# Performance work log

Hardware: AMD Instinct MI355X
Metric: run time of the kernel (lower is better)

Reference implementation:

```python
import jax, jax.numpy as jnp
import numpy as np

N, E, D, H, L = 50000, 800000, 64, 4, 2
DH = D // H


def layer_norm(h, g, b, eps=1e-5):
    mu = h.mean(-1, keepdims=True)
    var = ((h - mu) ** 2).mean(-1, keepdims=True)
    return (h - mu) / jnp.sqrt(var + eps) * g + b


def setup_inputs() -> dict:
    key = jax.random.key(0)
    ks = jax.random.split(key, 16)
    s = 1.0 / np.sqrt(D)
    inp = {
        "x": jax.random.normal(ks[0], (N, D), jnp.float32),
        "edge_attr": jax.random.normal(ks[1], (E, D), jnp.float32),
        "edge_index": jax.random.randint(ks[2], (2, E), 0, N, jnp.int64),
        "WQ": jax.random.normal(ks[3], (L, D, D), jnp.float32) * s,
        "WK": jax.random.normal(ks[4], (L, D, D), jnp.float32) * s,
        "WE": jax.random.normal(ks[5], (L, D, D), jnp.float32) * s,
        "WV": jax.random.normal(ks[6], (L, D, D), jnp.float32) * s,
        "WO": jax.random.normal(ks[7], (L, D, D), jnp.float32) * s,
        "bO": jnp.zeros((L, D), jnp.float32),
        "ln1_g": jnp.ones((L, D), jnp.float32),
        "ln1_b": jnp.zeros((L, D), jnp.float32),
        "W1": jax.random.normal(ks[8], (L, D, 2 * D), jnp.float32) * s,
        "b1": jnp.zeros((L, 2 * D), jnp.float32),
        "W2": jax.random.normal(ks[9], (L, 2 * D, D), jnp.float32) * (1.0 / np.sqrt(2 * D)),
        "b2": jnp.zeros((L, D), jnp.float32),
        "ln2_g": jnp.ones((L, D), jnp.float32),
        "ln2_b": jnp.zeros((L, D), jnp.float32),
    }
    return inp


def exphormer_layer(h, edge_attr, src, dst, p):
    (wq, wk, we, wv, wo, bo, g1, be1, w1, b1, w2, b2, g2, be2) = p
    n = h.shape[0]
    Qh = (h @ wq).reshape(n, H, DH)
    Kh = (h @ wk).reshape(n, H, DH)
    Vh = (h @ wv).reshape(n, H, DH)
    Eh = (edge_attr @ we).reshape(-1, H, DH)
    # per-edge score: sum over head_dim of K[src]*Q[dst]*E / sqrt(DH)
    s = jnp.sum(Kh[src] * Qh[dst] * Eh, axis=-1, keepdims=True) / np.sqrt(DH)
    score = jnp.exp(jnp.clip(s, -5.0, 5.0))  # [E, H, 1]
    msg = Vh[src] * score                     # [E, H, DH]
    wV = jax.ops.segment_sum(msg, dst, num_segments=n)    # [N, H, DH]
    Z = jax.ops.segment_sum(score, dst, num_segments=n)   # [N, H, 1]
    h_attn = (wV / (Z + 1e-6)).reshape(n, D)
    h1 = layer_norm(h + (h_attn @ wo + bo), g1, be1)
    ffn = jax.nn.relu(h1 @ w1 + b1) @ w2 + b2
    return layer_norm(h1 + ffn, g2, be2)


def reference(x, edge_attr, edge_index, WQ, WK, WE, WV, WO, bO, ln1_g, ln1_b,
              W1, b1, W2, b2, ln2_g, ln2_b):
    src = edge_index[0]
    dst = edge_index[1]
    h = x
    for l in range(L):
        p = (WQ[l], WK[l], WE[l], WV[l], WO[l], bO[l], ln1_g[l], ln1_b[l],
             W1[l], b1[l], W2[l], b2[l], ln2_g[l], ln2_b[l])
        h = exphormer_layer(h, edge_attr, src, dst, p)
    return h
```

## Files before the change

### kernel.cpp

```cpp
#include <hip/hip_runtime.h>

#define NN 50000
#define NE 800000
#define D  64
#define NL 2
#define NB 196

typedef __bf16 bf16x8 __attribute__((ext_vector_type(8)));
typedef float  floatx4 __attribute__((ext_vector_type(4)));

static __device__ __forceinline__ float bf2f(unsigned short u) {
    return __uint_as_float(((unsigned)u) << 16);
}
static __device__ __forceinline__ unsigned short f2bf(float x) {
    unsigned u = __float_as_uint(x);
    u += 0x7fff + ((u >> 16) & 1);
    return (unsigned short)(u >> 16);
}


__global__ void k_deg(const int* __restrict__ ei, int* __restrict__ deg) {
    int e = blockIdx.x * 256 + threadIdx.x;
    if (e < NE) atomicAdd(&deg[ei[NE + e]], 1);
}

__global__ __launch_bounds__(256) void k_scan1(const int* __restrict__ deg,
                                               int* __restrict__ psum) {
    __shared__ int red[4];
    int i = blockIdx.x * 256 + threadIdx.x;
    int v = (i < NN) ? deg[i] : 0;
#pragma unroll
    for (int m = 1; m < 64; m <<= 1) v += __shfl_xor(v, m, 64);
    if ((threadIdx.x & 63) == 0) red[threadIdx.x >> 6] = v;
    __syncthreads();
    if (threadIdx.x == 0) psum[blockIdx.x] = red[0] + red[1] + red[2] + red[3];
}

__global__ void k_scan2(int* __restrict__ psum) {
    __shared__ int buf[256];
    int t = threadIdx.x;
    int v = (t < NB) ? psum[t] : 0;
    buf[t] = v;
    __syncthreads();
    for (int o = 1; o < 256; o <<= 1) {
        int x = (t >= o) ? buf[t - o] : 0;
        __syncthreads();
        buf[t] += x;
        __syncthreads();
    }
    if (t < NB) psum[t] = buf[t] - v;
}

__global__ __launch_bounds__(256) void k_scan3(const int* __restrict__ deg,
                                               const int* __restrict__ psum,
                                               int* __restrict__ row_off,
                                               int* __restrict__ cursor) {
    __shared__ int buf[256];
    int t = threadIdx.x;
    int i = blockIdx.x * 256 + t;
    int v = (i < NN) ? deg[i] : 0;
    buf[t] = v;
    __syncthreads();
    for (int o = 1; o < 256; o <<= 1) {
        int x = (t >= o) ? buf[t - o] : 0;
        __syncthreads();
        buf[t] += x;
        __syncthreads();
    }
    if (i < NN) {
        int inc = buf[t] + psum[blockIdx.x];
        row_off[i + 1] = inc;
        cursor[i] = inc - v;
        if (i == 0) row_off[0] = 0;
    }
}

__global__ void k_scatter(const int* __restrict__ ei, int* __restrict__ cursor,
                          int* __restrict__ csr_src, int* __restrict__ eperm) {
    int e = blockIdx.x * 256 + threadIdx.x;
    if (e < NE) {
        int dst = ei[NE + e];
        int pos = atomicAdd(&cursor[dst], 1);
        csr_src[pos] = ei[e];
        eperm[e] = pos;
    }
}

__global__ __launch_bounds__(256) void k_prep(
        const float* __restrict__ WQ, const float* __restrict__ WK,
        const float* __restrict__ WV, const float* __restrict__ WE,
        const float* __restrict__ WO, const float* __restrict__ W1,
        const float* __restrict__ W2,
        unsigned short* __restrict__ wqT, unsigned short* __restrict__ wkT,
        unsigned short* __restrict__ wvT, unsigned short* __restrict__ weT,
        unsigned short* __restrict__ woT, unsigned short* __restrict__ w1T,
        unsigned short* __restrict__ w2T) {
    int idx = blockIdx.x * 256 + threadIdx.x;
    if (idx >= 2 * 36864) return;
    int l = idx / 36864;
    int r = idx % 36864;
    if (r < 20480) {
        int which = r >> 12, rr = r & 4095;
        int m = rr >> 6, k = rr & 63;
        const float* src = (which == 0 ? WQ : which == 1 ? WK : which == 2 ? WV :
                            which == 3 ? WE : WO);
        unsigned short* dst = (which == 0 ? wqT : which == 1 ? wkT : which == 2 ? wvT :
                               which == 3 ? weT : woT);
        dst[l * 4096 + rr] = f2bf(src[l * 4096 + k * 64 + m]);
    } else if (r < 28672) {
        int r2 = r - 20480;
        int m = r2 >> 6, k = r2 & 63;
        w1T[l * 8192 + r2] = f2bf(W1[l * 8192 + k * 128 + m]);
    } else {
        int r3 = r - 28672;
        int m = r3 >> 7, k = r3 & 127;
        w2T[l * 8192 + r3] = f2bf(W2[l * 8192 + k * 64 + m]);
    }
}


__global__ __launch_bounds__(256) void k_qkv_mfma(const float* __restrict__ h,
        const unsigned short* __restrict__ wqT, const unsigned short* __restrict__ wkT,
        const unsigned short* __restrict__ wvT,
        unsigned short* __restrict__ Qb, unsigned short* __restrict__ Kb,
        unsigned short* __restrict__ Vb) {
    __shared__ unsigned short st[4][16 * 72];
    const int lane = threadIdx.x & 63;
    const int w    = threadIdx.x >> 6;
    const int ml   = lane & 15;
    const int quad = lane >> 4;

    bf16x8 aq[2][4], ak[2][4], av[2][4];
#pragma unroll
    for (int kt = 0; kt < 2; kt++)
#pragma unroll
        for (int mt = 0; mt < 4; mt++) {
            int o = (mt*16 + ml)*64 + kt*32 + quad*8;
            aq[kt][mt] = *(const bf16x8*)&wqT[o];
            ak[kt][mt] = *(const bf16x8*)&wkT[o];
            av[kt][mt] = *(const bf16x8*)&wvT[o];
        }

    const int wave = blockIdx.x * 4 + w;
    const int nw   = gridDim.x * 4;
    const int el = lane >> 2, c = lane & 3;
    for (int tile = wave; tile < NN / 16; tile += nw) {
        const int e0 = tile * 16;
        const float4* ar = (const float4*)(h + (size_t)(e0 + ml) * D);
        bf16x8 b[2];
#pragma unroll
        for (int kt = 0; kt < 2; kt++) {
            float4 f0 = ar[kt*8 + quad*2 + 0];
            float4 f1 = ar[kt*8 + quad*2 + 1];
            b[kt][0] = (__bf16)f0.x; b[kt][1] = (__bf16)f0.y;
            b[kt][2] = (__bf16)f0.z; b[kt][3] = (__bf16)f0.w;
            b[kt][4] = (__bf16)f1.x; b[kt][5] = (__bf16)f1.y;
            b[kt][6] = (__bf16)f1.z; b[kt][7] = (__bf16)f1.w;
        }
        floatx4 accq[4] = {}, acck[4] = {}, accv[4] = {};
#pragma unroll
        for (int kt = 0; kt < 2; kt++)
#pragma unroll
            for (int mt = 0; mt < 4; mt++) {
                accq[mt] = __builtin_amdgcn_mfma_f32_16x16x32_bf16(aq[kt][mt], b[kt], accq[mt], 0, 0, 0);
                acck[mt] = __builtin_amdgcn_mfma_f32_16x16x32_bf16(ak[kt][mt], b[kt], acck[mt], 0, 0, 0);
                accv[mt] = __builtin_amdgcn_mfma_f32_16x16x32_bf16(av[kt][mt], b[kt], accv[mt], 0, 0, 0);
            }
#pragma unroll
        for (int mt = 0; mt < 4; mt++)
            *(ushort4*)&st[w][ml*72 + mt*16 + quad*4] =
                make_ushort4(f2bf(accq[mt][0]), f2bf(accq[mt][1]),
                             f2bf(accq[mt][2]), f2bf(accq[mt][3]));
        {
            uint4 r0 = *(const uint4*)&st[w][el*72 + c*16 + 0];
            uint4 r1 = *(const uint4*)&st[w][el*72 + c*16 + 8];
            uint4* gp = (uint4*)(Qb + (size_t)(e0 + el) * D + c*16);
            gp[0] = r0; gp[1] = r1;
        }
#pragma unroll
        for (int mt = 0; mt < 4; mt++)
            *(ushort4*)&st[w][ml*72 + mt*16 + quad*4] =
                make_ushort4(f2bf(acck[mt][0]), f2bf(acck[mt][1]),
                             f2bf(acck[mt][2]), f2bf(acck[mt][3]));
        {
            uint4 r0 = *(const uint4*)&st[w][el*72 + c*16 + 0];
            uint4 r1 = *(const uint4*)&st[w][el*72 + c*16 + 8];
            uint4* gp = (uint4*)(Kb + (size_t)(e0 + el) * D + c*16);
            gp[0] = r0; gp[1] = r1;
        }
#pragma unroll
        for (int mt = 0; mt < 4; mt++)
            *(ushort4*)&st[w][ml*72 + mt*16 + quad*4] =
                make_ushort4(f2bf(accv[mt][0]), f2bf(accv[mt][1]),
                             f2bf(accv[mt][2]), f2bf(accv[mt][3]));
        {
            uint4 r0 = *(const uint4*)&st[w][el*72 + c*16 + 0];
            uint4 r1 = *(const uint4*)&st[w][el*72 + c*16 + 8];
            uint4* gp = (uint4*)(Vb + (size_t)(e0 + el) * D + c*16);
            gp[0] = r0; gp[1] = r1;
        }
    }
}

__global__ __launch_bounds__(256) void k_eh_score(const float* __restrict__ ea,
        const unsigned short* __restrict__ weT, const int* __restrict__ eperm,
        const int* __restrict__ ei, const unsigned short* __restrict__ Qb,
        const unsigned short* __restrict__ Kb,
        float* __restrict__ scb, unsigned short* __restrict__ Eh1) {
    __shared__ unsigned short wsm[2 * 4608];
    __shared__ unsigned short st[4][16 * 72];
    const int t = threadIdx.x;
    for (int i = t; i < 1024; i += 256) {
        int l = i >> 9, r = i & 511;
        *(uint4*)&wsm[l*4608 + (r >> 3)*72 + (r & 7)*8] = ((const uint4*)weT)[i];
    }
    __syncthreads();

    const int lane = t & 63;
    const int w    = t >> 6;
    const int ml   = lane & 15;
    const int quad = lane >> 4;
    const int el = lane >> 2, c = lane & 3;
    const int wave = blockIdx.x * 4 + w;
    const int nw   = gridDim.x * 4;
    const int NT   = NE / 16;

    int tile = wave;
    if (tile >= NT) return;
    int srcn = ei[tile*16 + ml];
    int dstn = ei[NE + tile*16 + ml];
    int posm = eperm[tile*16 + ml];

    for (; tile < NT; tile += nw) {
        const float4* ar = (const float4*)(ea + (size_t)(tile*16 + ml) * D);
        float4 f00 = ar[quad*2 + 0];
        float4 f01 = ar[quad*2 + 1];
        float4 f10 = ar[8 + quad*2 + 0];
        float4 f11 = ar[8 + quad*2 + 1];
        ushort4 qg[4], kg[4];
#pragma unroll
        for (int mt = 0; mt < 4; mt++) {
            qg[mt] = *(const ushort4*)(Qb + (size_t)dstn * D + mt*16 + quad*4);
            kg[mt] = *(const ushort4*)(Kb + (size_t)srcn * D + mt*16 + quad*4);
        }
        int nxt = tile + nw;
        int nsrc = srcn, ndst = dstn, nposm = posm;
        if (nxt < NT) {
            nsrc  = ei[nxt*16 + ml];
            ndst  = ei[NE + nxt*16 + ml];
            nposm = eperm[nxt*16 + ml];
        }
        bf16x8 b[2];
        b[0][0] = (__bf16)f00.x; b[0][1] = (__bf16)f00.y;
        b[0][2] = (__bf16)f00.z; b[0][3] = (__bf16)f00.w;
        b[0][4] = (__bf16)f01.x; b[0][5] = (__bf16)f01.y;
        b[0][6] = (__bf16)f01.z; b[0][7] = (__bf16)f01.w;
        b[1][0] = (__bf16)f10.x; b[1][1] = (__bf16)f10.y;
        b[1][2] = (__bf16)f10.z; b[1][3] = (__bf16)f10.w;
        b[1][4] = (__bf16)f11.x; b[1][5] = (__bf16)f11.y;
        b[1][6] = (__bf16)f11.z; b[1][7] = (__bf16)f11.w;

        {
            floatx4 acc[4] = {};
#pragma unroll
            for (int kt = 0; kt < 2; kt++)
#pragma unroll
                for (int mt = 0; mt < 4; mt++) {
                    bf16x8 a = *(const bf16x8*)&wsm[4608 + (mt*16 + ml)*72 + kt*32 + quad*8];
                    acc[mt] = __builtin_amdgcn_mfma_f32_16x16x32_bf16(a, b[kt], acc[mt], 0, 0, 0);
                }
#pragma unroll
            for (int mt = 0; mt < 4; mt++)
                *(ushort4*)&st[w][ml*72 + mt*16 + quad*4] =
                    make_ushort4(f2bf(acc[mt][0]), f2bf(acc[mt][1]),
                                 f2bf(acc[mt][2]), f2bf(acc[mt][3]));
            uint4 r0 = *(const uint4*)&st[w][el*72 + c*16 + 0];
            uint4 r1 = *(const uint4*)&st[w][el*72 + c*16 + 8];
            uint4* gp = (uint4*)(Eh1 + (size_t)(tile*16 + el) * D + c*16);
            gp[0] = r0;
            gp[1] = r1;
        }
        {
            floatx4 acc[4] = {};
#pragma unroll
            for (int kt = 0; kt < 2; kt++)
#pragma unroll
                for (int mt = 0; mt < 4; mt++) {
                    bf16x8 a = *(const bf16x8*)&wsm[(mt*16 + ml)*72 + kt*32 + quad*8];
                    acc[mt] = __builtin_amdgcn_mfma_f32_16x16x32_bf16(a, b[kt], acc[mt], 0, 0, 0);
                }
            float scq[4];
#pragma unroll
            for (int mt = 0; mt < 4; mt++) {
                float p = acc[mt][0] * bf2f(qg[mt].x) * bf2f(kg[mt].x)
                        + acc[mt][1] * bf2f(qg[mt].y) * bf2f(kg[mt].y)
                        + acc[mt][2] * bf2f(qg[mt].z) * bf2f(kg[mt].z)
                        + acc[mt][3] * bf2f(qg[mt].w) * bf2f(kg[mt].w);
                p += __shfl_xor(p, 16, 64);
                p += __shfl_xor(p, 32, 64);
                scq[mt] = __expf(fminf(5.f, fmaxf(-5.f, p * 0.25f)));
            }
            if (quad == 0)
                *(float4*)(scb + (size_t)posm * 4) =
                    make_float4(scq[0], scq[1], scq[2], scq[3]);
        }
        srcn = nsrc; dstn = ndst; posm = nposm;
    }
}

__global__ __launch_bounds__(256) void k_score1(
        const unsigned short* __restrict__ Eh1,
        const unsigned short* __restrict__ Qb, const unsigned short* __restrict__ Kb,
        const int* __restrict__ ei, const int* __restrict__ eperm,
        float* __restrict__ scb) {
    const int lane = threadIdx.x & 63;
    const int w    = threadIdx.x >> 6;
    const int ml   = lane & 15;
    const int quad = lane >> 4;
    const int wave = blockIdx.x * 4 + w;
    const int nw   = gridDim.x * 4;
    const int NT   = NE / 16;
    int tile = wave;
    if (tile >= NT) return;
    int p0 = tile*16 + ml;
    int src = ei[p0], dst = ei[NE + p0], pos = eperm[p0];
    bf16x8 e0 = *(const bf16x8*)(Eh1 + (size_t)p0 * D + quad*16);
    bf16x8 e1 = *(const bf16x8*)(Eh1 + (size_t)p0 * D + quad*16 + 8);
    for (; tile < NT; tile += nw) {
        bf16x8 k0 = *(const bf16x8*)(Kb + (size_t)src * D + quad*16);
        bf16x8 k1 = *(const bf16x8*)(Kb + (size_t)src * D + quad*16 + 8);
        bf16x8 q0 = *(const bf16x8*)(Qb + (size_t)dst * D + quad*16);
        bf16x8 q1 = *(const bf16x8*)(Qb + (size_t)dst * D + quad*16 + 8);
        int nxt = tile + nw;
        int nsrc = src, ndst = dst, npos = pos;
        bf16x8 ne0 = e0, ne1 = e1;
        if (nxt < NT) {
            int pn = nxt*16 + ml;
            nsrc = ei[pn]; ndst = ei[NE + pn]; npos = eperm[pn];
            ne0 = *(const bf16x8*)(Eh1 + (size_t)pn * D + quad*16);
            ne1 = *(const bf16x8*)(Eh1 + (size_t)pn * D + quad*16 + 8);
        }
        float s = 0.f;
#pragma unroll
        for (int i = 0; i < 8; i++) s += (float)e0[i] * (float)q0[i] * (float)k0[i];
#pragma unroll
        for (int i = 0; i < 8; i++) s += (float)e1[i] * (float)q1[i] * (float)k1[i];
        scb[(size_t)pos * 4 + quad] = __expf(fminf(5.f, fmaxf(-5.f, s * 0.25f)));
        src = nsrc; dst = ndst; pos = npos; e0 = ne0; e1 = ne1;
    }
}

__global__ __launch_bounds__(256) void k_agg(
        const unsigned short* __restrict__ Vb, const float* __restrict__ scb,
        const int* __restrict__ row_off, const int* __restrict__ csr_src,
        unsigned short* __restrict__ h_attn) {
    const int node = blockIdx.x * 4 + (threadIdx.x >> 6);
    if (node >= NN) return;
    const int lane  = threadIdx.x & 63;
    const int eslot = lane >> 4;
    const int ml    = lane & 15;
    const int hsel  = ml >> 2;
    const int beg = row_off[node], end = row_off[node + 1];
    float4 acc = make_float4(0.f, 0.f, 0.f, 0.f);
    float z = 0.f;

    for (int cbeg = beg; cbeg < end; cbeg += 64) {
        const int cnt = min(64, end - cbeg);
        int myidx = cbeg + lane;
        int mysrc = (myidx < end) ? csr_src[myidx] : 0;

        for (int base = 0; base < cnt; base += 16) {
            int  jj[4];
            int  s[4];
            bool act[4];
#pragma unroll
            for (int u = 0; u < 4; u++) {
                int j = base + eslot + 4 * u;
                act[u] = j < cnt;
                jj[u]  = act[u] ? j : 0;
                s[u]   = __shfl(mysrc, jj[u], 64);
            }
            ushort4 vb[4];
            float   sv[4];
#pragma unroll
            for (int u = 0; u < 4; u++) {
                vb[u] = *(const ushort4*)(Vb + (size_t)s[u] * D + ml * 4);
                sv[u] = scb[(size_t)(cbeg + jj[u]) * 4 + hsel];
            }
#pragma unroll
            for (int u = 0; u < 4; u++) {
                float sc = act[u] ? sv[u] : 0.f;
                acc.x += sc * bf2f(vb[u].x);
                acc.y += sc * bf2f(vb[u].y);
                acc.z += sc * bf2f(vb[u].z);
                acc.w += sc * bf2f(vb[u].w);
                z += sc;
            }
        }
    }
#pragma unroll
    for (int m = 16; m <= 32; m <<= 1) {
        acc.x += __shfl_xor(acc.x, m, 64);
        acc.y += __shfl_xor(acc.y, m, 64);
        acc.z += __shfl_xor(acc.z, m, 64);
        acc.w += __shfl_xor(acc.w, m, 64);
        z     += __shfl_xor(z, m, 64);
    }
    if (eslot == 0) {
        float inv = 1.f / (z + 1e-6f);
        *(ushort4*)&h_attn[(size_t)node * D + ml * 4] =
            make_ushort4(f2bf(acc.x * inv), f2bf(acc.y * inv),
                         f2bf(acc.z * inv), f2bf(acc.w * inv));
    }
}

__global__ __launch_bounds__(512) void k_post_mfma(const float* __restrict__ h_in,
        const unsigned short* __restrict__ h_attn,
        const unsigned short* __restrict__ woT_g,
        const unsigned short* __restrict__ w1T_g,
        const unsigned short* __restrict__ w2T_g,
        const float* __restrict__ bo,
        const float* __restrict__ g1, const float* __restrict__ be1,
        const float* __restrict__ b1, const float* __restrict__ b2,
        const float* __restrict__ g2, const float* __restrict__ be2,
        float* __restrict__ h_out) {
    __shared__ unsigned short woT_s[64 * 72];
    __shared__ unsigned short w1T_s[128 * 72];
    __shared__ unsigned short w2T_s[64 * 136];
    __shared__ unsigned short stg[8][16 * 136];

    const int t = threadIdx.x;
    {
        const uint4* s0 = (const uint4*)woT_g;
        { int i = t; if (i < 512) { int row = i >> 3, c = i & 7;
              *(uint4*)&woT_s[row*72 + c*8] = s0[i]; } }
        const uint4* s1 = (const uint4*)w1T_g;
        for (int i = t; i < 1024; i += 512) {
            int row = i >> 3, c = i & 7;
            *(uint4*)&w1T_s[row*72 + c*8] = s1[i];
        }
        const uint4* s2 = (const uint4*)w2T_g;
        for (int i = t; i < 1024; i += 512) {
            int row = i >> 4, c = i & 15;
            *(uint4*)&w2T_s[row*136 + c*8] = s2[i];
        }
    }
    __syncthreads();

    const int w = t >> 6, lane = t & 63;
    const int ml = lane & 15, quad = lane >> 4;
    const int tile = blockIdx.x * 8 + w;
    if (tile >= NN / 16) return;
    const int e0 = tile * 16;
    unsigned short* st = stg[w];

    floatx4 acc1[4] = {};
#pragma unroll
    for (int kt = 0; kt < 2; kt++) {
        bf16x8 b = *(const bf16x8*)(h_attn + (size_t)(e0 + ml) * D + kt*32 + quad*8);
#pragma unroll
        for (int mt = 0; mt < 4; mt++) {
            bf16x8 a = *(const bf16x8*)&woT_s[(mt*16 + ml)*72 + kt*32 + quad*8];
            acc1[mt] = __builtin_amdgcn_mfma_f32_16x16x32_bf16(a, b, acc1[mt], 0, 0, 0);
        }
    }
    const float4* hp  = (const float4*)(h_in + (size_t)(e0 + ml) * D);
    const float4* bo4 = (const float4*)bo;
    floatx4 tt[4];
#pragma unroll
    for (int mt = 0; mt < 4; mt++) {
        float4 hh = hp[mt*4 + quad];
        float4 bb = bo4[mt*4 + quad];
        tt[mt][0] = acc1[mt][0] + hh.x + bb.x;
        tt[mt][1] = acc1[mt][1] + hh.y + bb.y;
        tt[mt][2] = acc1[mt][2] + hh.z + bb.z;
        tt[mt][3] = acc1[mt][3] + hh.w + bb.w;
    }
    float s = 0.f;
#pragma unroll
    for (int mt = 0; mt < 4; mt++) s += tt[mt][0] + tt[mt][1] + tt[mt][2] + tt[mt][3];
    s += __shfl_xor(s, 16, 64); s += __shfl_xor(s, 32, 64);
    float mu = s * (1.f / 64.f);
    float v = 0.f;
#pragma unroll
    for (int mt = 0; mt < 4; mt++)
#pragma unroll
        for (int r = 0; r < 4; r++) { float c = tt[mt][r] - mu; v += c * c; }
    v += __shfl_xor(v, 16, 64); v += __shfl_xor(v, 32, 64);
    float rstd = rsqrtf(v * (1.f / 64.f) + 1e-5f);
    const float4* g1v  = (const float4*)g1;
    const float4* be1v = (const float4*)be1;
    floatx4 h1[4];
#pragma unroll
    for (int mt = 0; mt < 4; mt++) {
        float4 gg = g1v[mt*4 + quad];
        float4 bb = be1v[mt*4 + quad];
        h1[mt][0] = (tt[mt][0] - mu) * rstd * gg.x + bb.x;
        h1[mt][1] = (tt[mt][1] - mu) * rstd * gg.y + bb.y;
        h1[mt][2] = (tt[mt][2] - mu) * rstd * gg.z + bb.z;
        h1[mt][3] = (tt[mt][3] - mu) * rstd * gg.w + bb.w;
        *(ushort4*)&st[ml*136 + mt*16 + quad*4] =
            make_ushort4(f2bf(h1[mt][0]), f2bf(h1[mt][1]), f2bf(h1[mt][2]), f2bf(h1[mt][3]));
    }

    bf16x8 bh[2];
#pragma unroll
    for (int kt = 0; kt < 2; kt++)
        bh[kt] = *(const bf16x8*)&st[ml*136 + kt*32 + quad*8];
    floatx4 acc2[8] = {};
#pragma unroll
    for (int kt = 0; kt < 2; kt++)
#pragma unroll
        for (int mt = 0; mt < 8; mt++) {
            bf16x8 a = *(const bf16x8*)&w1T_s[(mt*16 + ml)*72 + kt*32 + quad*8];
            acc2[mt] = __builtin_amdgcn_mfma_f32_16x16x32_bf16(a, bh[kt], acc2[mt], 0, 0, 0);
        }
    const float4* b1v = (const float4*)b1;
#pragma unroll
    for (int mt = 0; mt < 8; mt++) {
        float4 bb = b1v[mt*4 + quad];
        float y0 = fmaxf(acc2[mt][0] + bb.x, 0.f);
        float y1 = fmaxf(acc2[mt][1] + bb.y, 0.f);
        float y2 = fmaxf(acc2[mt][2] + bb.z, 0.f);
        float y3 = fmaxf(acc2[mt][3] + bb.w, 0.f);
        *(ushort4*)&st[ml*136 + mt*16 + quad*4] =
            make_ushort4(f2bf(y0), f2bf(y1), f2bf(y2), f2bf(y3));
    }

    floatx4 acc3[4] = {};
#pragma unroll
    for (int kt = 0; kt < 4; kt++) {
        bf16x8 b = *(const bf16x8*)&st[ml*136 + kt*32 + quad*8];
#pragma unroll
        for (int mt = 0; mt < 4; mt++) {
            bf16x8 a = *(const bf16x8*)&w2T_s[(mt*16 + ml)*136 + kt*32 + quad*8];
            acc3[mt] = __builtin_amdgcn_mfma_f32_16x16x32_bf16(a, b, acc3[mt], 0, 0, 0);
        }
    }
    const float4* b2v = (const float4*)b2;
#pragma unroll
    for (int mt = 0; mt < 4; mt++) {
        float4 bb = b2v[mt*4 + quad];
        tt[mt][0] = acc3[mt][0] + bb.x + h1[mt][0];
        tt[mt][1] = acc3[mt][1] + bb.y + h1[mt][1];
        tt[mt][2] = acc3[mt][2] + bb.z + h1[mt][2];
        tt[mt][3] = acc3[mt][3] + bb.w + h1[mt][3];
    }
    s = 0.f;
#pragma unroll
    for (int mt = 0; mt < 4; mt++) s += tt[mt][0] + tt[mt][1] + tt[mt][2] + tt[mt][3];
    s += __shfl_xor(s, 16, 64); s += __shfl_xor(s, 32, 64);
    mu = s * (1.f / 64.f);
    v = 0.f;
#pragma unroll
    for (int mt = 0; mt < 4; mt++)
#pragma unroll
        for (int r = 0; r < 4; r++) { float c = tt[mt][r] - mu; v += c * c; }
    v += __shfl_xor(v, 16, 64); v += __shfl_xor(v, 32, 64);
    rstd = rsqrtf(v * (1.f / 64.f) + 1e-5f);
    const float4* g2v  = (const float4*)g2;
    const float4* be2v = (const float4*)be2;
    float4* outp = (float4*)(h_out + (size_t)(e0 + ml) * D);
#pragma unroll
    for (int mt = 0; mt < 4; mt++) {
        float4 gg = g2v[mt*4 + quad];
        float4 bb = be2v[mt*4 + quad];
        float4 o;
        o.x = (tt[mt][0] - mu) * rstd * gg.x + bb.x;
        o.y = (tt[mt][1] - mu) * rstd * gg.y + bb.y;
        o.z = (tt[mt][2] - mu) * rstd * gg.z + bb.z;
        o.w = (tt[mt][3] - mu) * rstd * gg.w + bb.w;
        outp[mt*4 + quad] = o;
    }
}


extern "C" void kernel_launch(void* const* d_in, const int* in_sizes, int n_in,
                              void* d_out, int out_size, void* d_ws, size_t ws_size,
                              hipStream_t stream) {
    const float* x   = (const float*)d_in[0];
    const float* ea  = (const float*)d_in[1];
    const int*   ei  = (const int*)d_in[2];
    const float* WQ  = (const float*)d_in[3];
    const float* WK  = (const float*)d_in[4];
    const float* WE  = (const float*)d_in[5];
    const float* WV  = (const float*)d_in[6];
    const float* WO  = (const float*)d_in[7];
    const float* bO  = (const float*)d_in[8];
    const float* g1  = (const float*)d_in[9];
    const float* be1 = (const float*)d_in[10];
    const float* W1  = (const float*)d_in[11];
    const float* b1  = (const float*)d_in[12];
    const float* W2  = (const float*)d_in[13];
    const float* b2  = (const float*)d_in[14];
    const float* g2  = (const float*)d_in[15];
    const float* be2 = (const float*)d_in[16];
    float* out = (float*)d_out;

    char* wsb = (char*)d_ws;
    size_t off = 0;
    auto alloc = [&](size_t bytes) {
        void* p = wsb + off;
        off += (bytes + 255) & ~(size_t)255;
        return p;
    };
    unsigned short* Qb   = (unsigned short*)alloc((size_t)NN * D * 2);
    unsigned short* Kb   = (unsigned short*)alloc((size_t)NN * D * 2);
    unsigned short* Vb   = (unsigned short*)alloc((size_t)NN * D * 2);
    float* hbuf          = (float*)alloc((size_t)NN * D * 4);
    unsigned short* hattn= (unsigned short*)alloc((size_t)NN * D * 2);
    unsigned short* Eh1  = (unsigned short*)alloc((size_t)NE * D * 2);
    float* scb           = (float*)alloc((size_t)NE * 4 * 4);
    int* row_off         = (int*)alloc((size_t)(NN + 1) * 4);
    int* cursor          = (int*)alloc((size_t)NN * 4);
    int* deg             = (int*)alloc((size_t)NN * 4);
    int* psum            = (int*)alloc((size_t)256 * 4);
    int* csr_src         = (int*)alloc((size_t)NE * 4);
    int* eperm           = (int*)alloc((size_t)NE * 4);
    unsigned short* wqT  = (unsigned short*)alloc((size_t)2 * 4096 * 2);
    unsigned short* wkT  = (unsigned short*)alloc((size_t)2 * 4096 * 2);
    unsigned short* wvT  = (unsigned short*)alloc((size_t)2 * 4096 * 2);
    unsigned short* weT  = (unsigned short*)alloc((size_t)2 * 4096 * 2);
    unsigned short* woT  = (unsigned short*)alloc((size_t)2 * 4096 * 2);
    unsigned short* w1T  = (unsigned short*)alloc((size_t)2 * 8192 * 2);
    unsigned short* w2T  = (unsigned short*)alloc((size_t)2 * 8192 * 2);

    hipMemsetAsync(deg, 0, (size_t)NN * 4, stream);
    k_deg<<<(NE + 255) / 256, 256, 0, stream>>>(ei, deg);
    k_scan1<<<NB, 256, 0, stream>>>(deg, psum);
    k_scan2<<<1, 256, 0, stream>>>(psum);
    k_scan3<<<NB, 256, 0, stream>>>(deg, psum, row_off, cursor);
    k_scatter<<<(NE + 255) / 256, 256, 0, stream>>>(ei, cursor, csr_src, eperm);
    k_prep<<<(2 * 36864 + 255) / 256, 256, 0, stream>>>(WQ, WK, WV, WE, WO, W1, W2,
            wqT, wkT, wvT, weT, woT, w1T, w2T);

    k_qkv_mfma<<<782, 256, 0, stream>>>(x, wqT, wkT, wvT, Qb, Kb, Vb);
    k_eh_score<<<1280, 256, 0, stream>>>(ea, weT, eperm, ei, Qb, Kb, scb, Eh1);

    k_agg<<<(NN + 3) / 4, 256, 0, stream>>>(Vb, scb, row_off, csr_src, hattn);
    k_post_mfma<<<(NN / 16 + 7) / 8, 512, 0, stream>>>(x, hattn,
            woT, w1T, w2T, bO, g1, be1, b1, b2, g2, be2, hbuf);

    k_qkv_mfma<<<782, 256, 0, stream>>>(hbuf, wqT + 4096, wkT + 4096,
                                        wvT + 4096, Qb, Kb, Vb);
    k_score1<<<1536, 256, 0, stream>>>(Eh1, Qb, Kb, ei, eperm, scb);
    k_agg<<<(NN + 3) / 4, 256, 0, stream>>>(Vb, scb, row_off, csr_src, hattn);
    k_post_mfma<<<(NN / 16 + 7) / 8, 512, 0, stream>>>(hbuf, hattn,
            woT + 4096, w1T + 8192, w2T + 8192,
            bO + 64, g1 + 64, be1 + 64, b1 + 128, b2 + 64,
            g2 + 64, be2 + 64, out);
}
```

Before: 622.2 us.

## Prefetch edge attrs, widen Q/K/V gathers to 16-byte loads in score and agg

The fused edge-score kernel now software-prefetches the next tile's edge_attr rows along with the indices. It computes scores per (edge, head) from LDS-staged E projections, with Q/K gathered as 16-byte bf16x8 loads instead of several 8-byte loads. The aggregation kernel handles 8 edges per wave step with 8 lanes each loading 8 bf16 of V, instead of 4 edges with 16 lanes loading 4 values. This cuts the number of gather instructions and hides edge_attr load latency, at the cost of more registers and an extra LDS round trip plus bf16 rounding of the E projection.

After: 614.2 us. Within noise of the previous version (-1.3%).

```diff
diff --git a/kernel.cpp b/kernel.cpp
--- a/kernel.cpp
+++ b/kernel.cpp
@@ -227,28 +227,32 @@
 
     int tile = wave;
     if (tile >= NT) return;
-    int srcn = ei[tile*16 + ml];
-    int dstn = ei[NE + tile*16 + ml];
-    int posm = eperm[tile*16 + ml];
+    int srce = ei[tile*16 + el];
+    int dste = ei[NE + tile*16 + el];
+    int pose = eperm[tile*16 + el];
+    const float4* ar0 = (const float4*)(ea + (size_t)(tile*16 + ml) * D);
+    float4 f00 = ar0[quad*2 + 0];
+    float4 f01 = ar0[quad*2 + 1];
+    float4 f10 = ar0[8 + quad*2 + 0];
+    float4 f11 = ar0[8 + quad*2 + 1];
 
     for (; tile < NT; tile += nw) {
-        const float4* ar = (const float4*)(ea + (size_t)(tile*16 + ml) * D);
-        float4 f00 = ar[quad*2 + 0];
-        float4 f01 = ar[quad*2 + 1];
-        float4 f10 = ar[8 + quad*2 + 0];
-        float4 f11 = ar[8 + quad*2 + 1];
-        ushort4 qg[4], kg[4];
-#pragma unroll
-        for (int mt = 0; mt < 4; mt++) {
-            qg[mt] = *(const ushort4*)(Qb + (size_t)dstn * D + mt*16 + quad*4);
-            kg[mt] = *(const ushort4*)(Kb + (size_t)srcn * D + mt*16 + quad*4);
-        }
+        bf16x8 qg0 = *(const bf16x8*)(Qb + (size_t)dste * D + c*16);
+        bf16x8 qg1 = *(const bf16x8*)(Qb + (size_t)dste * D + c*16 + 8);
+        bf16x8 kg0 = *(const bf16x8*)(Kb + (size_t)srce * D + c*16);
+        bf16x8 kg1 = *(const bf16x8*)(Kb + (size_t)srce * D + c*16 + 8);
         int nxt = tile + nw;
-        int nsrc = srcn, ndst = dstn, nposm = posm;
+        float4 nf00 = f00, nf01 = f01, nf10 = f10, nf11 = f11;
+        int nsrc = srce, ndst = dste, npos = pose;
         if (nxt < NT) {
-            nsrc  = ei[nxt*16 + ml];
-            ndst  = ei[NE + nxt*16 + ml];
-            nposm = eperm[nxt*16 + ml];
+            const float4* ar = (const float4*)(ea + (size_t)(nxt*16 + ml) * D);
+            nf00 = ar[quad*2 + 0];
+            nf01 = ar[quad*2 + 1];
+            nf10 = ar[8 + quad*2 + 0];
+            nf11 = ar[8 + quad*2 + 1];
+            nsrc = ei[nxt*16 + el];
+            ndst = ei[NE + nxt*16 + el];
+            npos = eperm[nxt*16 + el];
         }
         bf16x8 b[2];
         b[0][0] = (__bf16)f00.x; b[0][1] = (__bf16)f00.y;
@@ -289,22 +293,22 @@
                     bf16x8 a = *(const bf16x8*)&wsm[(mt*16 + ml)*72 + kt*32 + quad*8];
                     acc[mt] = __builtin_amdgcn_mfma_f32_16x16x32_bf16(a, b[kt], acc[mt], 0, 0, 0);
                 }
-            float scq[4];
-#pragma unroll
-            for (int mt = 0; mt < 4; mt++) {
-                float p = acc[mt][0] * bf2f(qg[mt].x) * bf2f(kg[mt].x)
-                        + acc[mt][1] * bf2f(qg[mt].y) * bf2f(kg[mt].y)
-                        + acc[mt][2] * bf2f(qg[mt].z) * bf2f(kg[mt].z)
-                        + acc[mt][3] * bf2f(qg[mt].w) * bf2f(kg[mt].w);
-                p += __shfl_xor(p, 16, 64);
-                p += __shfl_xor(p, 32, 64);
-                scq[mt] = __expf(fminf(5.f, fmaxf(-5.f, p * 0.25f)));
-            }
-            if (quad == 0)
-                *(float4*)(scb + (size_t)posm * 4) =
-                    make_float4(scq[0], scq[1], scq[2], scq[3]);
-        }
-        srcn = nsrc; dstn = ndst; posm = nposm;
+#pragma unroll
+            for (int mt = 0; mt < 4; mt++)
+                *(ushort4*)&st[w][ml*72 + mt*16 + quad*4] =
+                    make_ushort4(f2bf(acc[mt][0]), f2bf(acc[mt][1]),
+                                 f2bf(acc[mt][2]), f2bf(acc[mt][3]));
+            bf16x8 e0v = *(const bf16x8*)&st[w][el*72 + c*16];
+            bf16x8 e1v = *(const bf16x8*)&st[w][el*72 + c*16 + 8];
+            float s = 0.f;
+#pragma unroll
+            for (int i = 0; i < 8; i++) s += (float)e0v[i] * (float)qg0[i] * (float)kg0[i];
+#pragma unroll
+            for (int i = 0; i < 8; i++) s += (float)e1v[i] * (float)qg1[i] * (float)kg1[i];
+            scb[(size_t)pose * 4 + c] = __expf(fminf(5.f, fmaxf(-5.f, s * 0.25f)));
+        }
+        f00 = nf00; f01 = nf01; f10 = nf10; f11 = nf11;
+        srce = nsrc; dste = ndst; pose = npos;
     }
 }
 
@@ -357,11 +361,11 @@
     const int node = blockIdx.x * 4 + (threadIdx.x >> 6);
     if (node >= NN) return;
     const int lane  = threadIdx.x & 63;
-    const int eslot = lane >> 4;
-    const int ml    = lane & 15;
-    const int hsel  = ml >> 2;
+    const int eslot = lane >> 3;
+    const int ml    = lane & 7;
+    const int head  = ml >> 1;
     const int beg = row_off[node], end = row_off[node + 1];
-    float4 acc = make_float4(0.f, 0.f, 0.f, 0.f);
+    floatx4 a0 = {}, a1 = {};
     float z = 0.f;
 
     for (int cbeg = beg; cbeg < end; cbeg += 64) {
@@ -370,47 +374,54 @@
         int mysrc = (myidx < end) ? csr_src[myidx] : 0;
 
         for (int base = 0; base < cnt; base += 16) {
-            int  jj[4];
-            int  s[4];
-            bool act[4];
-#pragma unroll
-            for (int u = 0; u < 4; u++) {
-                int j = base + eslot + 4 * u;
+            int  jj[2];
+            int  s[2];
+            bool act[2];
+#pragma unroll
+            for (int u = 0; u < 2; u++) {
+                int j = base + eslot + 8 * u;
                 act[u] = j < cnt;
                 jj[u]  = act[u] ? j : 0;
                 s[u]   = __shfl(mysrc, jj[u], 64);
             }
-            ushort4 vb[4];
-            float   sv[4];
-#pragma unroll
-            for (int u = 0; u < 4; u++) {
-                vb[u] = *(const ushort4*)(Vb + (size_t)s[u] * D + ml * 4);
-                sv[u] = scb[(size_t)(cbeg + jj[u]) * 4 + hsel];
+            bf16x8 vb[2];
+            float  sv[2];
+#pragma unroll
+            for (int u = 0; u < 2; u++) {
+                vb[u] = *(const bf16x8*)(Vb + (size_t)s[u] * D + ml * 8);
+                sv[u] = scb[(size_t)(cbeg + jj[u]) * 4 + head];
             }
 #pragma unroll
-            for (int u = 0; u < 4; u++) {
+            for (int u = 0; u < 2; u++) {
                 float sc = act[u] ? sv[u] : 0.f;
-                acc.x += sc * bf2f(vb[u].x);
-                acc.y += sc * bf2f(vb[u].y);
-                acc.z += sc * bf2f(vb[u].z);
-                acc.w += sc * bf2f(vb[u].w);
+                a0[0] += sc * (float)vb[u][0];
+                a0[1] += sc * (float)vb[u][1];
+                a0[2] += sc * (float)vb[u][2];
+                a0[3] += sc * (float)vb[u][3];
+                a1[0] += sc * (float)vb[u][4];
+                a1[1] += sc * (float)vb[u][5];
+                a1[2] += sc * (float)vb[u][6];
+                a1[3] += sc * (float)vb[u][7];
                 z += sc;
             }
         }
     }
 #pragma unroll
-    for (int m = 16; m <= 32; m <<= 1) {
-        acc.x += __shfl_xor(acc.x, m, 64);
-        acc.y += __shfl_xor(acc.y, m, 64);
-        acc.z += __shfl_xor(acc.z, m, 64);
-        acc.w += __shfl_xor(acc.w, m, 64);
-        z     += __shfl_xor(z, m, 64);
+    for (int m = 8; m <= 32; m <<= 1) {
+#pragma unroll
+        for (int r = 0; r < 4; r++) {
+            a0[r] += __shfl_xor(a0[r], m, 64);
+            a1[r] += __shfl_xor(a1[r], m, 64);
+        }
+        z += __shfl_xor(z, m, 64);
     }
     if (eslot == 0) {
         float inv = 1.f / (z + 1e-6f);
-        *(ushort4*)&h_attn[(size_t)node * D + ml * 4] =
-            make_ushort4(f2bf(acc.x * inv), f2bf(acc.y * inv),
-                         f2bf(acc.z * inv), f2bf(acc.w * inv));
+        unsigned r0 = ((unsigned)f2bf(a0[1] * inv) << 16) | f2bf(a0[0] * inv);
+        unsigned r1 = ((unsigned)f2bf(a0[3] * inv) << 16) | f2bf(a0[2] * inv);
+        unsigned r2 = ((unsigned)f2bf(a1[1] * inv) << 16) | f2bf(a1[0] * inv);
+        unsigned r3 = ((unsigned)f2bf(a1[3] * inv) << 16) | f2bf(a1[2] * inv);
+        *(uint4*)&h_attn[(size_t)node * D + ml * 8] = make_uint4(r0, r1, r2, r3);
     }
 }
 
```
